# Kernel tuning notes

Measured on AMD Instinct MI355X. Metric: run time of the kernel, lower is better.

The kernel has to match this reference:

```python
import jax, jax.numpy as jnp
import numpy as np

IMG = 2048
STRIDES = [8, 16, 32, 64, 128]
A = 9                       # num_cell_anchors
CLASS_NUM = 16              # num_classes - 1
TOPK = 1000                 # config.test_layer_topk
MAX_DELTA = float(np.log(1000.0 / 16.0))

_LEVEL_N = [(IMG // s) * (IMG // s) * A for s in STRIDES]


def setup_inputs() -> dict:
    key = jax.random.key(0)
    inp = {}
    for l, n in enumerate(_LEVEL_N):
        key, k1, k2, k3, k4 = jax.random.split(key, 5)
        cxcy = jax.random.uniform(k1, (n, 2), minval=0.0, maxval=float(IMG))
        wh = jax.random.uniform(k2, (n, 2), minval=8.0, maxval=128.0)
        inp[f"anchors{l}"] = jnp.concatenate([cxcy - 0.5 * wh, cxcy + 0.5 * wh], axis=1)
        # logits biased negative like a trained RetinaNet cls head (prior_prob init)
        inp[f"cls{l}"] = jax.random.normal(k3, (1, n, CLASS_NUM), dtype=jnp.float32) - 4.0
        inp[f"reg{l}"] = jax.random.normal(k4, (1, n, 8), dtype=jnp.float32) * 0.1
    return inp


def bbox_transform_inv(rois, deltas):
    # standard box decode (restore_bbox with unnormalize=False)
    w = rois[:, 2] - rois[:, 0]
    h = rois[:, 3] - rois[:, 1]
    cx = rois[:, 0] + 0.5 * w
    cy = rois[:, 1] + 0.5 * h
    pcx = cx + deltas[:, 0] * w
    pcy = cy + deltas[:, 1] * h
    pw = w * jnp.exp(jnp.minimum(deltas[:, 2], MAX_DELTA))
    ph = h * jnp.exp(jnp.minimum(deltas[:, 3], MAX_DELTA))
    return jnp.stack([pcx - 0.5 * pw, pcy - 0.5 * ph,
                      pcx + 0.5 * pw, pcy + 0.5 * ph], axis=1)


def _per_layer(anchors, pred_cls, pred_reg):
    a = anchors.reshape(-1, 4)
    c = pred_cls[0].reshape(-1, CLASS_NUM)
    r = pred_reg[0].reshape(-1, 8)[:, :4]
    if a.shape[0] > TOPK:
        ruler = jnp.max(c, axis=1)                  # max score over classes
        _, inds = jax.lax.top_k(ruler, TOPK)        # irregular topk + gather
        a = jnp.take(a, inds, axis=0)
        c = jnp.take(c, inds, axis=0)
        r = jnp.take(r, inds, axis=0)
    return a, jax.nn.sigmoid(c), r


def reference(anchors0, cls0, reg0, anchors1, cls1, reg1, anchors2, cls2, reg2,
              anchors3, cls3, reg3, anchors4, cls4, reg4):
    levels = [(anchors0, cls0, reg0), (anchors1, cls1, reg1),
              (anchors2, cls2, reg2), (anchors3, cls3, reg3),
              (anchors4, cls4, reg4)]
    kept = [_per_layer(a, c, r) for a, c, r in levels]
    keep_anchors = jnp.concatenate([k[0] for k in kept], axis=0)   # [K,4]
    keep_cls = jnp.concatenate([k[1] for k in kept], axis=0)       # [K,C]
    keep_reg = jnp.concatenate([k[2] for k in kept], axis=0)       # [K,4]
    K = keep_cls.shape[0]
    tag = jnp.tile(jnp.arange(CLASS_NUM, dtype=keep_cls.dtype) + 1.0, (K,)).reshape(-1, 1)
    pred_scores = keep_cls.reshape(-1, 1)                          # [K*C,1]
    pred_bbox = bbox_transform_inv(keep_anchors, keep_reg)         # [K,4]
    pred_bbox = jnp.tile(pred_bbox, (1, CLASS_NUM)).reshape(-1, 4) # [K*C,4]
    return jnp.concatenate([pred_bbox, pred_scores, tag], axis=1)  # [K*C,6]
```

## Files before the change

### kernel.cpp

```cpp
#include <hip/hip_runtime.h>
#include <math.h>

#define NLEV 5
#define TOPKK 1000
#define NCLS 16
#define NPART 16
#define HP 16u
#define PART_CAP 256
#define CAND_TOT 2048
#define NCHUNK 3069u
#define HISTSZ (NLEV * 256)
#define BAR_STRIDE 2048u

__device__ __forceinline__ unsigned g_load(const unsigned* p) {
    return __hip_atomic_load(p, __ATOMIC_RELAXED, __HIP_MEMORY_SCOPE_AGENT);
}
__device__ __forceinline__ unsigned long long g_load64(const unsigned long long* p) {
    return __hip_atomic_load(p, __ATOMIC_RELAXED, __HIP_MEMORY_SCOPE_AGENT);
}
__device__ __forceinline__ void g_store(unsigned* p, unsigned v) {
    __hip_atomic_store(p, v, __ATOMIC_RELAXED, __HIP_MEMORY_SCOPE_AGENT);
}
__device__ __forceinline__ void g_store64(unsigned long long* p, unsigned long long v) {
    __hip_atomic_store(p, v, __ATOMIC_RELAXED, __HIP_MEMORY_SCOPE_AGENT);
}

__device__ __forceinline__ int lev_of_chunk(unsigned c) {
    if (c < 2304u) return 0;
    if (c < 2880u) return 1;
    if (c < 3024u) return 2;
    if (c < 3060u) return 3;
    return 4;
}
__device__ __forceinline__ unsigned lev_base(int l) {
    unsigned b = 0u;
    if (l == 1) b = 589824u;
    if (l == 2) b = 737280u;
    if (l == 3) b = 774144u;
    if (l == 4) b = 783360u;
    return b;
}

struct Ptrs {
    const float* anc[NLEV];
    const float* cls[NLEV];
    const float* reg[NLEV];
};

__device__ __forceinline__ unsigned f2key(float f) {
    unsigned u = __float_as_uint(f);
    return (u & 0x80000000u) ? ~u : (u | 0x80000000u);
}

__device__ __forceinline__ float max4(float4 v) {
    return fmaxf(fmaxf(v.x, v.y), fmaxf(v.z, v.w));
}

__device__ __forceinline__ void bar_arrive(unsigned* inst) {
    if (threadIdx.x == 0) g_store(inst + blockIdx.x, 1u);
}

template<unsigned NBV>
__device__ __forceinline__ void bar_monitor_fanout(unsigned* inst, unsigned* wsh) {
    constexpr unsigned W = (NBV + 255u) / 256u;
    for (;;) {
        bool all = true;
        #pragma unroll
        for (unsigned i = 0; i < W; i++) {
            unsigned idx = i * 256u + (unsigned)threadIdx.x;
            unsigned f = (idx < NBV) ? g_load(inst + idx) : 1u;
            all = all && (f != 0u);
        }
        unsigned long long bal = __ballot(all);
        if ((threadIdx.x & 63) == 0)
            wsh[threadIdx.x >> 6] = (bal == 0xFFFFFFFFFFFFFFFFull) ? 1u : 0u;
        __syncthreads();
        bool done = wsh[0] && wsh[1] && wsh[2] && wsh[3];
        __syncthreads();
        if (done) break;
        __builtin_amdgcn_s_sleep(2);
    }
    if (threadIdx.x < 16)
        g_store(inst + 1024u + (unsigned)threadIdx.x * 16u, 1u);
}

__device__ __forceinline__ void bar_waitgo(unsigned* inst) {
    unsigned g = blockIdx.x & 15u;
    while (!g_load(inst + 1024u + g * 16u))
        __builtin_amdgcn_s_sleep(4);
}

template<unsigned NBV>
__device__ __forceinline__ void gridbar(unsigned* inst, unsigned* wsh) {
    __syncthreads();
    bar_arrive(inst);
    if (blockIdx.x == 0) {
        bar_monitor_fanout<NBV>(inst, wsh);
    } else if (threadIdx.x == 0) {
        bar_waitgo(inst);
    }
    __syncthreads();
}

__device__ __forceinline__ void sel256(unsigned c, unsigned rem,
                                       unsigned* wsum, unsigned* aux) {
    int t = threadIdx.x, lane = t & 63, wv = t >> 6;
    unsigned s = c;
    #pragma unroll
    for (int d = 1; d < 64; d <<= 1) {
        unsigned o = __shfl_down(s, d, 64);
        if (lane + d < 64) s += o;
    }
    if (lane == 0) wsum[wv] = s;
    __syncthreads();
    unsigned incl = s;
    #pragma unroll
    for (int w2 = 1; w2 < 4; w2++) if (wv + w2 < 4) incl += wsum[wv + w2];
    unsigned above = incl - c;
    if (above < rem && rem <= incl) {
        aux[0] = (unsigned)t;
        aux[1] = rem - above;
    }
    __syncthreads();
}

template<unsigned CPBV, unsigned NBV>
__global__ __launch_bounds__(256, 2) void k_fused(Ptrs p, unsigned* histA,
        unsigned* histB, unsigned* cnt, unsigned* bar,
        unsigned long long* cand, float* out) {
    __shared__ unsigned long long lbuf[CAND_TOT];
    __shared__ unsigned hh[256];
    __shared__ unsigned wsum[4];
    __shared__ unsigned wsh[4];
    __shared__ unsigned aux[33];

    const unsigned b = blockIdx.x;
    const int t = threadIdx.x;
    const unsigned c0 = b * CPBV;
    const int lev = lev_of_chunk(c0);
    const unsigned ebase = lev_base(lev);
    unsigned* bar0 = bar;
    unsigned* bar1 = bar + BAR_STRIDE;
    unsigned* bar2 = bar + 2u * BAR_STRIDE;

    unsigned keys[CPBV];
    #pragma unroll
    for (unsigned j = 0; j < CPBV; j++) {
        unsigned ch = c0 + j;
        unsigned k = 0u;
        if (ch < NCHUNK) {
            unsigned loc = ch * 256u + (unsigned)t - ebase;
            const float4* cp = (const float4*)(p.cls[lev]) + (size_t)loc * 4;
            float4 v0 = cp[0], v1 = cp[1], v2 = cp[2], v3 = cp[3];
            float m = fmaxf(fmaxf(max4(v0), max4(v1)), fmaxf(max4(v2), max4(v3)));
            k = f2key(m);
        }
        keys[j] = k;
    }
    hh[t] = 0u;
    __syncthreads();
    #pragma unroll
    for (unsigned j = 0; j < CPBV; j++)
        if (c0 + j < NCHUNK) atomicAdd(&hh[keys[j] >> 24], 1u);
    __syncthreads();
    {
        unsigned v = hh[t];
        if (v) atomicAdd(&histA[(b & (HP - 1u)) * HISTSZ
                                + (unsigned)lev * 256u + (unsigned)t], v);
    }
    gridbar<NBV>(bar0, wsh);

    unsigned cA = 0;
    #pragma unroll
    for (unsigned pp = 0; pp < HP; pp++)
        cA += g_load(histA + pp * HISTSZ + (unsigned)lev * 256u + (unsigned)t);
    sel256(cA, TOPKK, wsum, aux);
    unsigned binA = aux[0], remA = aux[1];
    __syncthreads();

    hh[t] = 0u;
    __syncthreads();
    #pragma unroll
    for (unsigned j = 0; j < CPBV; j++) {
        unsigned k = keys[j];
        if ((c0 + j) < NCHUNK && (k >> 24) == binA)
            atomicAdd(&hh[(k >> 16) & 0xFFu], 1u);
    }
    __syncthreads();
    {
        unsigned v = hh[t];
        if (v) atomicAdd(&histB[(b & (HP - 1u)) * HISTSZ
                                + (unsigned)lev * 256u + (unsigned)t], v);
    }
    gridbar<NBV>(bar1, wsh);

    unsigned cB = 0;
    #pragma unroll
    for (unsigned pp = 0; pp < HP; pp++)
        cB += g_load(histB + pp * HISTSZ + (unsigned)lev * 256u + (unsigned)t);
    sel256(cB, remA, wsum, aux);
    unsigned thresh = (binA << 24) | (aux[0] << 16);
    __syncthreads();

    #pragma unroll
    for (unsigned j = 0; j < CPBV; j++) {
        unsigned ch = c0 + j;
        unsigned k = keys[j];
        if (ch < NCHUNK && k >= thresh) {
            unsigned loc = ch * 256u + (unsigned)t - ebase;
            unsigned part = ch & (NPART - 1u);
            unsigned slot = atomicAdd(&cnt[(lev * NPART + part) * 16u], 1u);
            if (slot < PART_CAP)
                g_store64(&cand[((size_t)(lev * NPART + part)) * PART_CAP + slot],
                          ((unsigned long long)k << 32) | (unsigned)(~loc));
        }
    }

    bool ranker = b < (unsigned)(NLEV * 8);
    __syncthreads();
    bar_arrive(bar2);
    if (b == 0) {
        bar_monitor_fanout<NBV>(bar2, wsh);
    } else if (ranker) {
        if (t == 0) bar_waitgo(bar2);
    } else {
        return;
    }
    __syncthreads();

    const float MAXD = 4.135166556742356f;
    int l = (int)(b >> 3);
    unsigned sl = b & 7u;

    if (t < NPART) {
        unsigned cc = g_load(cnt + (l * NPART + t) * 16u);
        aux[t] = (cc > PART_CAP) ? PART_CAP : cc;
    }
    __syncthreads();
    if (t == 0) {
        unsigned o = 0;
        for (int pp = 0; pp < NPART; pp++) { aux[16 + pp] = o; o += aux[pp]; }
        aux[32] = (o > CAND_TOT) ? CAND_TOT : o;
    }
    __syncthreads();
    unsigned n = aux[32];
    for (int pp = 0; pp < NPART; pp++) {
        unsigned cc = aux[pp], o = aux[16 + pp];
        for (unsigned e = (unsigned)t; e < cc; e += 256u) {
            unsigned dst = o + e;
            if (dst < CAND_TOT)
                lbuf[dst] = g_load64(&cand[((size_t)(l * NPART + pp)) * PART_CAP + e]);
        }
    }
    __syncthreads();

    unsigned j = sl * 256u + (unsigned)t;
    if (j >= n) return;
    unsigned long long my = lbuf[j];
    unsigned rank = 0;
    #pragma unroll 8
    for (unsigned q = 0; q < n; q++) rank += (lbuf[q] > my) ? 1u : 0u;
    if (rank >= TOPKK) return;

    unsigned idx = ~((unsigned)(my & 0xFFFFFFFFull));
    float4 an = ((const float4*)p.anc[l])[idx];
    float4 dd = ((const float4*)p.reg[l])[(size_t)idx * 2];
    float w = an.z - an.x, h = an.w - an.y;
    float cx = an.x + 0.5f * w, cy = an.y + 0.5f * h;
    float pcx = cx + dd.x * w, pcy = cy + dd.y * h;
    float pw = w * expf(fminf(dd.z, MAXD));
    float ph = h * expf(fminf(dd.w, MAXD));
    float bx = pcx - 0.5f * pw, by = pcy - 0.5f * ph;
    float bz = pcx + 0.5f * pw, bw = pcy + 0.5f * ph;

    const float4* cp = (const float4*)(p.cls[l]) + (size_t)idx * 4;
    float sg[16];
    #pragma unroll
    for (int g = 0; g < 4; g++) {
        float4 v = cp[g];
        sg[4 * g + 0] = 1.0f / (1.0f + expf(-v.x));
        sg[4 * g + 1] = 1.0f / (1.0f + expf(-v.y));
        sg[4 * g + 2] = 1.0f / (1.0f + expf(-v.z));
        sg[4 * g + 3] = 1.0f / (1.0f + expf(-v.w));
    }
    float4* q = (float4*)(out + (size_t)(l * TOPKK + rank) * (NCLS * 6));
    #pragma unroll
    for (int g = 0; g < 8; g++) {
        float ta = (float)(2 * g + 1), tb = (float)(2 * g + 2);
        q[3 * g + 0] = make_float4(bx, by, bz, bw);
        q[3 * g + 1] = make_float4(sg[2 * g], ta, bx, by);
        q[3 * g + 2] = make_float4(bz, bw, sg[2 * g + 1], tb);
    }
}

extern "C" void kernel_launch(void* const* d_in, const int* in_sizes, int n_in,
                              void* d_out, int out_size, void* d_ws, size_t ws_size,
                              hipStream_t stream) {
    (void)in_sizes; (void)n_in; (void)out_size; (void)ws_size;
    Ptrs p;
    for (int l = 0; l < NLEV; l++) {
        p.anc[l] = (const float*)d_in[3 * l + 0];
        p.cls[l] = (const float*)d_in[3 * l + 1];
        p.reg[l] = (const float*)d_in[3 * l + 2];
    }

    static int s_which = -1;
    if (s_which < 0) {
        int bpcu = 0;
        if (hipOccupancyMaxActiveBlocksPerMultiprocessor(
                &bpcu, (const void*)k_fused<3u, 1023u>, 256, 0) != hipSuccess)
            bpcu = 0;
        int dev = 0, ncu = 0;
        (void)hipGetDevice(&dev);
        if (hipDeviceGetAttribute(&ncu, hipDeviceAttributeMultiprocessorCount,
                                  dev) != hipSuccess || ncu < 1)
            ncu = 0;
        s_which = (bpcu >= 4 && (long long)bpcu * ncu >= 1023) ? 1 : 0;
    }

    char* w = (char*)d_ws;
    unsigned* histA = (unsigned*)w;
    unsigned* histB = (unsigned*)(w + 81920);
    unsigned* cnt   = (unsigned*)(w + 163840);
    unsigned* bar   = (unsigned*)(w + 168960);
    unsigned long long* cand = (unsigned long long*)(w + 193536);
    float* out = (float*)d_out;

    (void)hipMemsetAsync(w, 0, 193536, stream);
    if (s_which == 1) {
        k_fused<3u, 1023u><<<dim3(1023), dim3(256), 0, stream>>>(
            p, histA, histB, cnt, bar, cand, out);
    } else {
        k_fused<6u, 512u><<<dim3(512), dim3(256), 0, stream>>>(
            p, histA, histB, cnt, bar, cand, out);
    }
}
```

Measured before the change: 166.9 us.

## Replace grid-wide barriers with per-level counter barriers and add 1535-block config

Swaps the three grid-wide flag barriers, which block 0 monitors and then fans out, for per-level atomic counters. Each level's blocks now wait only for the blocks of their own level, and each waiter polls 16 striped counters. This is meant to cut barrier latency and stop small levels waiting on the large level-0 blocks. It also adds a 1535-block, 2-chunks-per-block launch variant, selected when occupancy allows, to raise parallelism. The counter polling adds atomic contention, and with more blocks, co-residency is required for the spin-waits to be safe.

```diff
diff --git a/kernel.cpp b/kernel.cpp
--- a/kernel.cpp
+++ b/kernel.cpp
@@ -10,16 +10,12 @@
 #define CAND_TOT 2048
 #define NCHUNK 3069u
 #define HISTSZ (NLEV * 256)
-#define BAR_STRIDE 2048u
 
 __device__ __forceinline__ unsigned g_load(const unsigned* p) {
     return __hip_atomic_load(p, __ATOMIC_RELAXED, __HIP_MEMORY_SCOPE_AGENT);
 }
 __device__ __forceinline__ unsigned long long g_load64(const unsigned long long* p) {
     return __hip_atomic_load(p, __ATOMIC_RELAXED, __HIP_MEMORY_SCOPE_AGENT);
-}
-__device__ __forceinline__ void g_store(unsigned* p, unsigned v) {
-    __hip_atomic_store(p, v, __ATOMIC_RELAXED, __HIP_MEMORY_SCOPE_AGENT);
 }
 __device__ __forceinline__ void g_store64(unsigned long long* p, unsigned long long v) {
     __hip_atomic_store(p, v, __ATOMIC_RELAXED, __HIP_MEMORY_SCOPE_AGENT);
@@ -40,6 +36,12 @@
     if (l == 4) b = 783360u;
     return b;
 }
+template<unsigned CPBV>
+__device__ __forceinline__ unsigned lev_expect(int l) {
+    unsigned lc = (l == 0) ? 2304u : (l == 1) ? 576u : (l == 2) ? 144u
+                : (l == 3) ? 36u : 9u;
+    return (lc + CPBV - 1u) / CPBV;
+}
 
 struct Ptrs {
     const float* anc[NLEV];
@@ -56,48 +58,22 @@
     return fmaxf(fmaxf(v.x, v.y), fmaxf(v.z, v.w));
 }
 
-__device__ __forceinline__ void bar_arrive(unsigned* inst) {
-    if (threadIdx.x == 0) g_store(inst + blockIdx.x, 1u);
-}
-
-template<unsigned NBV>
-__device__ __forceinline__ void bar_monitor_fanout(unsigned* inst, unsigned* wsh) {
-    constexpr unsigned W = (NBV + 255u) / 256u;
-    for (;;) {
-        bool all = true;
-        #pragma unroll
-        for (unsigned i = 0; i < W; i++) {
-            unsigned idx = i * 256u + (unsigned)threadIdx.x;
-            unsigned f = (idx < NBV) ? g_load(inst + idx) : 1u;
-            all = all && (f != 0u);
+__device__ __forceinline__ void lev_arrive(unsigned* sync, int round, int lev) {
+    if (threadIdx.x == 0)
+        atomicAdd(&sync[(unsigned)round * 1280u + (unsigned)lev * 256u
+                        + (blockIdx.x & 15u) * 16u], 1u);
+}
+__device__ __forceinline__ void lev_wait(unsigned* sync, int round, int lev,
+                                         unsigned expect) {
+    if (threadIdx.x == 0) {
+        const unsigned* p = sync + (unsigned)round * 1280u + (unsigned)lev * 256u;
+        for (;;) {
+            unsigned s = 0;
+            #pragma unroll
+            for (int i = 0; i < 16; i++) s += g_load(p + i * 16);
+            if (s == expect) break;
+            __builtin_amdgcn_s_sleep(2);
         }
-        unsigned long long bal = __ballot(all);
-        if ((threadIdx.x & 63) == 0)
-            wsh[threadIdx.x >> 6] = (bal == 0xFFFFFFFFFFFFFFFFull) ? 1u : 0u;
-        __syncthreads();
-        bool done = wsh[0] && wsh[1] && wsh[2] && wsh[3];
-        __syncthreads();
-        if (done) break;
-        __builtin_amdgcn_s_sleep(2);
-    }
-    if (threadIdx.x < 16)
-        g_store(inst + 1024u + (unsigned)threadIdx.x * 16u, 1u);
-}
-
-__device__ __forceinline__ void bar_waitgo(unsigned* inst) {
-    unsigned g = blockIdx.x & 15u;
-    while (!g_load(inst + 1024u + g * 16u))
-        __builtin_amdgcn_s_sleep(4);
-}
-
-template<unsigned NBV>
-__device__ __forceinline__ void gridbar(unsigned* inst, unsigned* wsh) {
-    __syncthreads();
-    bar_arrive(inst);
-    if (blockIdx.x == 0) {
-        bar_monitor_fanout<NBV>(inst, wsh);
-    } else if (threadIdx.x == 0) {
-        bar_waitgo(inst);
     }
     __syncthreads();
 }
@@ -126,12 +102,11 @@
 
 template<unsigned CPBV, unsigned NBV>
 __global__ __launch_bounds__(256, 2) void k_fused(Ptrs p, unsigned* histA,
-        unsigned* histB, unsigned* cnt, unsigned* bar,
+        unsigned* histB, unsigned* cnt, unsigned* sync,
         unsigned long long* cand, float* out) {
     __shared__ unsigned long long lbuf[CAND_TOT];
     __shared__ unsigned hh[256];
     __shared__ unsigned wsum[4];
-    __shared__ unsigned wsh[4];
     __shared__ unsigned aux[33];
 
     const unsigned b = blockIdx.x;
@@ -139,9 +114,7 @@
     const unsigned c0 = b * CPBV;
     const int lev = lev_of_chunk(c0);
     const unsigned ebase = lev_base(lev);
-    unsigned* bar0 = bar;
-    unsigned* bar1 = bar + BAR_STRIDE;
-    unsigned* bar2 = bar + 2u * BAR_STRIDE;
+    const unsigned expect = lev_expect<CPBV>(lev);
 
     unsigned keys[CPBV];
     #pragma unroll
@@ -168,7 +141,9 @@
         if (v) atomicAdd(&histA[(b & (HP - 1u)) * HISTSZ
                                 + (unsigned)lev * 256u + (unsigned)t], v);
     }
-    gridbar<NBV>(bar0, wsh);
+    __syncthreads();
+    lev_arrive(sync, 0, lev);
+    lev_wait(sync, 0, lev, expect);
 
     unsigned cA = 0;
     #pragma unroll
@@ -192,7 +167,9 @@
         if (v) atomicAdd(&histB[(b & (HP - 1u)) * HISTSZ
                                 + (unsigned)lev * 256u + (unsigned)t], v);
     }
-    gridbar<NBV>(bar1, wsh);
+    __syncthreads();
+    lev_arrive(sync, 1, lev);
+    lev_wait(sync, 1, lev, expect);
 
     unsigned cB = 0;
     #pragma unroll
@@ -215,21 +192,16 @@
                           ((unsigned long long)k << 32) | (unsigned)(~loc));
         }
     }
+    __syncthreads();
+    lev_arrive(sync, 2, lev);
 
     bool ranker = b < (unsigned)(NLEV * 8);
-    __syncthreads();
-    bar_arrive(bar2);
-    if (b == 0) {
-        bar_monitor_fanout<NBV>(bar2, wsh);
-    } else if (ranker) {
-        if (t == 0) bar_waitgo(bar2);
-    } else {
-        return;
-    }
-    __syncthreads();
+    if (!ranker) return;
+    int rl = (int)(b >> 3);
+    lev_wait(sync, 2, rl, lev_expect<CPBV>(rl));
 
     const float MAXD = 4.135166556742356f;
-    int l = (int)(b >> 3);
+    int l = rl;
     unsigned sl = b & 7u;
 
     if (t < NPART) {
@@ -308,30 +280,35 @@
     if (s_which < 0) {
         int bpcu = 0;
         if (hipOccupancyMaxActiveBlocksPerMultiprocessor(
-                &bpcu, (const void*)k_fused<3u, 1023u>, 256, 0) != hipSuccess)
+                &bpcu, (const void*)k_fused<2u, 1535u>, 256, 0) != hipSuccess)
             bpcu = 0;
         int dev = 0, ncu = 0;
         (void)hipGetDevice(&dev);
         if (hipDeviceGetAttribute(&ncu, hipDeviceAttributeMultiprocessorCount,
                                   dev) != hipSuccess || ncu < 1)
             ncu = 0;
-        s_which = (bpcu >= 4 && (long long)bpcu * ncu >= 1023) ? 1 : 0;
+        long long cap = (long long)bpcu * (long long)ncu;
+        s_which = (bpcu >= 6 && cap >= 1535) ? 2
+                : (bpcu >= 4 && cap >= 1023) ? 1 : 0;
     }
 
     char* w = (char*)d_ws;
     unsigned* histA = (unsigned*)w;
     unsigned* histB = (unsigned*)(w + 81920);
     unsigned* cnt   = (unsigned*)(w + 163840);
-    unsigned* bar   = (unsigned*)(w + 168960);
-    unsigned long long* cand = (unsigned long long*)(w + 193536);
+    unsigned* sync  = (unsigned*)(w + 168960);
+    unsigned long long* cand = (unsigned long long*)(w + 184320);
     float* out = (float*)d_out;
 
-    (void)hipMemsetAsync(w, 0, 193536, stream);
-    if (s_which == 1) {
+    (void)hipMemsetAsync(w, 0, 184320, stream);
+    if (s_which == 2) {
+        k_fused<2u, 1535u><<<dim3(1535), dim3(256), 0, stream>>>(
+            p, histA, histB, cnt, sync, cand, out);
+    } else if (s_which == 1) {
         k_fused<3u, 1023u><<<dim3(1023), dim3(256), 0, stream>>>(
-            p, histA, histB, cnt, bar, cand, out);
+            p, histA, histB, cnt, sync, cand, out);
     } else {
         k_fused<6u, 512u><<<dim3(512), dim3(256), 0, stream>>>(
-            p, histA, histB, cnt, bar, cand, out);
-    }
-}
+            p, histA, histB, cnt, sync, cand, out);
+    }
+}
```

Measured after the change: 192.5 us. +15.4%, slower.

## Use per-block barrier go flags, coalesced class loads, and batched candidate loads

Applied to the files above, without the earlier changes.

The grid barrier now gives each block its own go flag (stride 4) instead of 16 shared flags, and polls with shorter sleeps, to cut release latency and contention. The class-score pass now loads float4s coalesced across threads and reduces the per-anchor max with lane shuffles, which changes the anchor-to-thread mapping (eloc). Histogram partial sums and the candidate gather are restructured so all loads are issued before use, increasing memory-level parallelism. The workspace and memset grow to hold the larger barrier area, and block 0 now does more stores at release.

```diff
diff --git a/kernel.cpp b/kernel.cpp
--- a/kernel.cpp
+++ b/kernel.cpp
@@ -10,7 +10,7 @@
 #define CAND_TOT 2048
 #define NCHUNK 3069u
 #define HISTSZ (NLEV * 256)
-#define BAR_STRIDE 2048u
+#define BAR_U32 5120u
 
 __device__ __forceinline__ unsigned g_load(const unsigned* p) {
     return __hip_atomic_load(p, __ATOMIC_RELAXED, __HIP_MEMORY_SCOPE_AGENT);
@@ -62,32 +62,28 @@
 
 template<unsigned NBV>
 __device__ __forceinline__ void bar_monitor_fanout(unsigned* inst, unsigned* wsh) {
-    constexpr unsigned W = (NBV + 255u) / 256u;
+    const int t = threadIdx.x;
     for (;;) {
-        bool all = true;
-        #pragma unroll
-        for (unsigned i = 0; i < W; i++) {
-            unsigned idx = i * 256u + (unsigned)threadIdx.x;
-            unsigned f = (idx < NBV) ? g_load(inst + idx) : 1u;
-            all = all && (f != 0u);
-        }
-        unsigned long long bal = __ballot(all);
-        if ((threadIdx.x & 63) == 0)
-            wsh[threadIdx.x >> 6] = (bal == 0xFFFFFFFFFFFFFFFFull) ? 1u : 0u;
+        unsigned f0 = g_load(inst + t);
+        unsigned f1 = (256u + (unsigned)t < NBV) ? g_load(inst + 256 + t) : 1u;
+        unsigned f2 = (NBV > 512u && 512u + (unsigned)t < NBV) ? g_load(inst + 512 + t) : 1u;
+        unsigned f3 = (NBV > 768u && 768u + (unsigned)t < NBV) ? g_load(inst + 768 + t) : 1u;
+        unsigned all = f0 & f1 & f2 & f3;
+        unsigned long long bal = __ballot(all != 0u);
+        if ((t & 63) == 0) wsh[t >> 6] = (bal == 0xFFFFFFFFFFFFFFFFull) ? 1u : 0u;
         __syncthreads();
         bool done = wsh[0] && wsh[1] && wsh[2] && wsh[3];
         __syncthreads();
         if (done) break;
+        __builtin_amdgcn_s_sleep(1);
+    }
+    for (unsigned idx = (unsigned)t; idx < NBV; idx += 256u)
+        g_store(inst + 1024u + idx * 4u, 1u);
+}
+
+__device__ __forceinline__ void bar_waitgo(unsigned* inst) {
+    while (!g_load(inst + 1024u + blockIdx.x * 4u))
         __builtin_amdgcn_s_sleep(2);
-    }
-    if (threadIdx.x < 16)
-        g_store(inst + 1024u + (unsigned)threadIdx.x * 16u, 1u);
-}
-
-__device__ __forceinline__ void bar_waitgo(unsigned* inst) {
-    unsigned g = blockIdx.x & 15u;
-    while (!g_load(inst + 1024u + g * 16u))
-        __builtin_amdgcn_s_sleep(4);
 }
 
 template<unsigned NBV>
@@ -122,6 +118,18 @@
         aux[1] = rem - above;
     }
     __syncthreads();
+}
+
+__device__ __forceinline__ unsigned hist_sum(const unsigned* hist, int lev) {
+    unsigned vv[HP];
+    #pragma unroll
+    for (unsigned pp = 0; pp < HP; pp++)
+        vv[pp] = g_load(hist + pp * HISTSZ + (unsigned)lev * 256u
+                        + (unsigned)threadIdx.x);
+    unsigned s = 0;
+    #pragma unroll
+    for (unsigned pp = 0; pp < HP; pp++) s += vv[pp];
+    return s;
 }
 
 template<unsigned CPBV, unsigned NBV>
@@ -140,20 +148,33 @@
     const int lev = lev_of_chunk(c0);
     const unsigned ebase = lev_base(lev);
     unsigned* bar0 = bar;
-    unsigned* bar1 = bar + BAR_STRIDE;
-    unsigned* bar2 = bar + 2u * BAR_STRIDE;
+    unsigned* bar1 = bar + BAR_U32;
+    unsigned* bar2 = bar + 2u * BAR_U32;
 
     unsigned keys[CPBV];
+    const float4* f4p = (const float4*)(p.cls[lev]);
     #pragma unroll
     for (unsigned j = 0; j < CPBV; j++) {
         unsigned ch = c0 + j;
         unsigned k = 0u;
         if (ch < NCHUNK) {
-            unsigned loc = ch * 256u + (unsigned)t - ebase;
-            const float4* cp = (const float4*)(p.cls[lev]) + (size_t)loc * 4;
-            float4 v0 = cp[0], v1 = cp[1], v2 = cp[2], v3 = cp[3];
-            float m = fmaxf(fmaxf(max4(v0), max4(v1)), fmaxf(max4(v2), max4(v3)));
-            k = f2key(m);
+            unsigned base4 = (ch * 256u - ebase) * 4u;
+            float4 a0 = f4p[base4 + 0u * 256u + (unsigned)t];
+            float4 a1 = f4p[base4 + 1u * 256u + (unsigned)t];
+            float4 a2 = f4p[base4 + 2u * 256u + (unsigned)t];
+            float4 a3 = f4p[base4 + 3u * 256u + (unsigned)t];
+            float m0 = max4(a0), m1 = max4(a1), m2 = max4(a2), m3 = max4(a3);
+            m0 = fmaxf(m0, __shfl_xor(m0, 1, 64));
+            m0 = fmaxf(m0, __shfl_xor(m0, 2, 64));
+            m1 = fmaxf(m1, __shfl_xor(m1, 1, 64));
+            m1 = fmaxf(m1, __shfl_xor(m1, 2, 64));
+            m2 = fmaxf(m2, __shfl_xor(m2, 1, 64));
+            m2 = fmaxf(m2, __shfl_xor(m2, 2, 64));
+            m3 = fmaxf(m3, __shfl_xor(m3, 1, 64));
+            m3 = fmaxf(m3, __shfl_xor(m3, 2, 64));
+            int g = t & 3;
+            float mm = (g == 0) ? m0 : (g == 1) ? m1 : (g == 2) ? m2 : m3;
+            k = f2key(mm);
         }
         keys[j] = k;
     }
@@ -170,11 +191,7 @@
     }
     gridbar<NBV>(bar0, wsh);
 
-    unsigned cA = 0;
-    #pragma unroll
-    for (unsigned pp = 0; pp < HP; pp++)
-        cA += g_load(histA + pp * HISTSZ + (unsigned)lev * 256u + (unsigned)t);
-    sel256(cA, TOPKK, wsum, aux);
+    sel256(hist_sum(histA, lev), TOPKK, wsum, aux);
     unsigned binA = aux[0], remA = aux[1];
     __syncthreads();
 
@@ -194,20 +211,17 @@
     }
     gridbar<NBV>(bar1, wsh);
 
-    unsigned cB = 0;
-    #pragma unroll
-    for (unsigned pp = 0; pp < HP; pp++)
-        cB += g_load(histB + pp * HISTSZ + (unsigned)lev * 256u + (unsigned)t);
-    sel256(cB, remA, wsum, aux);
+    sel256(hist_sum(histB, lev), remA, wsum, aux);
     unsigned thresh = (binA << 24) | (aux[0] << 16);
     __syncthreads();
 
+    const unsigned eloc = (((unsigned)t & 3u) << 6) | ((unsigned)t >> 2);
     #pragma unroll
     for (unsigned j = 0; j < CPBV; j++) {
         unsigned ch = c0 + j;
         unsigned k = keys[j];
         if (ch < NCHUNK && k >= thresh) {
-            unsigned loc = ch * 256u + (unsigned)t - ebase;
+            unsigned loc = ch * 256u - ebase + eloc;
             unsigned part = ch & (NPART - 1u);
             unsigned slot = atomicAdd(&cnt[(lev * NPART + part) * 16u], 1u);
             if (slot < PART_CAP)
@@ -244,12 +258,22 @@
     }
     __syncthreads();
     unsigned n = aux[32];
-    for (int pp = 0; pp < NPART; pp++) {
-        unsigned cc = aux[pp], o = aux[16 + pp];
-        for (unsigned e = (unsigned)t; e < cc; e += 256u) {
-            unsigned dst = o + e;
-            if (dst < CAND_TOT)
-                lbuf[dst] = g_load64(&cand[((size_t)(l * NPART + pp)) * PART_CAP + e]);
+    {
+        unsigned long long tv[NPART];
+        unsigned vok = 0u;
+        #pragma unroll
+        for (int pp = 0; pp < NPART; pp++) {
+            bool ok = (unsigned)t < aux[pp];
+            if (ok) tv[pp] = g_load64(&cand[((size_t)(l * NPART + pp)) * PART_CAP
+                                            + (unsigned)t]);
+            vok |= ok ? (1u << pp) : 0u;
+        }
+        #pragma unroll
+        for (int pp = 0; pp < NPART; pp++) {
+            if (vok & (1u << pp)) {
+                unsigned dst = aux[16 + pp] + (unsigned)t;
+                if (dst < CAND_TOT) lbuf[dst] = tv[pp];
+            }
         }
     }
     __syncthreads();
@@ -323,10 +347,10 @@
     unsigned* histB = (unsigned*)(w + 81920);
     unsigned* cnt   = (unsigned*)(w + 163840);
     unsigned* bar   = (unsigned*)(w + 168960);
-    unsigned long long* cand = (unsigned long long*)(w + 193536);
+    unsigned long long* cand = (unsigned long long*)(w + 230400);
     float* out = (float*)d_out;
 
-    (void)hipMemsetAsync(w, 0, 193536, stream);
+    (void)hipMemsetAsync(w, 0, 230400, stream);
     if (s_which == 1) {
         k_fused<3u, 1023u><<<dim3(1023), dim3(256), 0, stream>>>(
             p, histA, histB, cnt, bar, cand, out);
```

New measurement: 163.4 us. 2.1% less time.
